# Performance work log

Measured on AMD Instinct MI355X. Metric: run time of the kernel, lower is better.

## Reference

```python
import jax, jax.numpy as jnp
import numpy as np

N_NODES = 10000
N_EDGES = 640000
IN_FEATS = 128
H_FEATS1 = 128
NUM_OUTPUTS = 64


def setup_inputs() -> dict:
    key = jax.random.key(0)
    k0, k1, k2, k3, k4 = jax.random.split(key, 5)
    in_feat = jax.random.normal(k0, (N_NODES, IN_FEATS), dtype=jnp.float32)
    src = jax.random.randint(k1, (N_EDGES,), 0, N_NODES, dtype=jnp.int64)
    dst = jax.random.randint(k2, (N_EDGES,), 0, N_NODES, dtype=jnp.int64)
    W1 = jax.random.normal(k3, (IN_FEATS, H_FEATS1), dtype=jnp.float32) * 0.05
    b1 = jnp.zeros((H_FEATS1,), dtype=jnp.float32)
    W2 = jax.random.normal(k4, (H_FEATS1, NUM_OUTPUTS), dtype=jnp.float32) * 0.05
    b2 = jnp.zeros((NUM_OUTPUTS,), dtype=jnp.float32)
    return {"in_feat": in_feat, "src": src, "dst": dst,
            "W1": W1, "b1": b1, "W2": W2, "b2": b2}


def _graph_conv(src, dst, x, W, b):
    # DGL GraphConv with norm='both': out = D_out^{-1/2} A^T-agg D_in^{-1/2} x W + b
    n = x.shape[0]
    ones = jnp.ones((src.shape[0],), dtype=x.dtype)
    deg_out = jnp.clip(jax.ops.segment_sum(ones, src, num_segments=n), 1.0)
    deg_in = jnp.clip(jax.ops.segment_sum(ones, dst, num_segments=n), 1.0)
    h = x * jax.lax.rsqrt(deg_out)[:, None]            # src-side normalization
    agg = jax.ops.segment_sum(h[src], dst, num_segments=n)  # SpMM: sum over in-edges
    agg = agg * jax.lax.rsqrt(deg_in)[:, None]         # dst-side normalization
    return agg @ W + b


def reference(in_feat, src, dst, W1, b1, W2, b2):
    h = _graph_conv(src, dst, in_feat, W1, b1)
    h = jax.nn.relu(h)  # dropout=0 -> identity
    return _graph_conv(src, dst, h, W2, b2)
```

## Files before the change

kernel.cpp:

```cpp
#include <hip/hip_runtime.h>
#include <hip/hip_fp16.h>

#define NFEAT 128
#define NOUT  64
#define PCAP  128
#define HB    256
#define NPB   16

__global__ void hist_kernel(const int* __restrict__ src, const int* __restrict__ dst,
                            unsigned char* __restrict__ hist_src,
                            unsigned char* __restrict__ hist_dst,
                            int nN, int nE) {
    extern __shared__ int bins[];
    int b = blockIdx.x;
    int per = (nE + HB - 1) / HB;
    int lo = b * per, hi = min(lo + per, nE);
    for (int i = threadIdx.x; i < nN; i += blockDim.x) bins[i] = 0;
    __syncthreads();
    for (int e = lo + threadIdx.x; e < hi; e += blockDim.x) {
        int s = src[e], d = dst[e];
        atomicAdd(&bins[d], 1);
        atomicAdd(&bins[s], 0x10000);
    }
    __syncthreads();
    for (int i = threadIdx.x; i < nN; i += blockDim.x) {
        int v = bins[i];
        hist_dst[(size_t)b * nN + i] = (unsigned char)min(v & 0xFFFF, 255);
        hist_src[(size_t)b * nN + i] = (unsigned char)min(v >> 16, 255);
    }
}

__global__ void offsets_kernel(const unsigned char* __restrict__ hist_src,
                               const unsigned char* __restrict__ hist_dst,
                               unsigned char* __restrict__ base_rel,
                               unsigned short* __restrict__ deg_in,
                               float* __restrict__ rs_in, float* __restrict__ rs_out, int nN) {
    int tid = blockIdx.x * blockDim.x + threadIdx.x;
    int wid = tid >> 6;
    int lane = tid & 63;
    int i0 = wid * 4;
    if (i0 >= nN) return;
    int c0 = lane * 4;
    unsigned int d[4], s4[4];
#pragma unroll
    for (int u = 0; u < 4; u++) {
        d[u]  = *(const unsigned int*)&hist_dst[(size_t)(c0 + u) * nN + i0];
        s4[u] = *(const unsigned int*)&hist_src[(size_t)(c0 + u) * nN + i0];
    }
    unsigned int run = 0, pre[4];
#pragma unroll
    for (int u = 0; u < 4; u++) { pre[u] = run; run += d[u]; }
    unsigned int ssum = s4[0] + s4[1] + s4[2] + s4[3];
    unsigned int inc = run;
#pragma unroll
    for (int off = 1; off < 64; off <<= 1) {
        unsigned int t = (unsigned int)__shfl_up((int)inc, off);
        if (lane >= off) inc += t;
    }
    unsigned int excl = inc - run;
#pragma unroll
    for (int u = 0; u < 4; u++)
        *(unsigned int*)&base_rel[(size_t)(c0 + u) * nN + i0] = excl + pre[u];
    unsigned int dtot = (unsigned int)__shfl((int)inc, 63);
#pragma unroll
    for (int off = 1; off < 64; off <<= 1)
        ssum += (unsigned int)__shfl_xor((int)ssum, off);
    if (lane < 4) {
        int i = i0 + lane;
        int dg = (dtot >> (8 * lane)) & 0xFF;
        int sg = (ssum >> (8 * lane)) & 0xFF;
        deg_in[i] = (unsigned short)min(dg, PCAP);
        rs_in[i]  = rsqrtf(fmaxf((float)dg, 1.0f));
        rs_out[i] = rsqrtf(fmaxf((float)sg, 1.0f));
    }
}

__global__ void scatter_kernel(const int* __restrict__ src, const int* __restrict__ dst,
                               const unsigned char* __restrict__ base_rel,
                               const float* __restrict__ x, const float* __restrict__ rs_out,
                               unsigned short* __restrict__ csr, uint4* __restrict__ xh,
                               int nN, int nE) {
    extern __shared__ int cur[];
    int b = blockIdx.x;
    int per = (nE + HB - 1) / HB;
    int lo = b * per, hi = min(lo + per, nE);
    for (int i = threadIdx.x; i < nN; i += blockDim.x)
        cur[i] = base_rel[(size_t)b * nN + i];
    __syncthreads();
    for (int e = lo + threadIdx.x; e < hi; e += blockDim.x) {
        int s = src[e], d = dst[e];
        int pos = atomicAdd(&cur[d], 1);
        if (pos < PCAP)
            csr[(size_t)d * PCAP + pos] = (unsigned short)s;
    }
    const float4* xf = (const float4*)x;
    int nchunk = nN * NFEAT / 8;
    for (int c = blockIdx.x * blockDim.x + threadIdx.x; c < nchunk; c += gridDim.x * blockDim.x) {
        int row = c >> 4;
        float rs = rs_out[row];
        float4 a = xf[2 * c], bb = xf[2 * c + 1];
        __half2 h[4] = {__floats2half2_rn(a.x * rs, a.y * rs),
                        __floats2half2_rn(a.z * rs, a.w * rs),
                        __floats2half2_rn(bb.x * rs, bb.y * rs),
                        __floats2half2_rn(bb.z * rs, bb.w * rs)};
        xh[c] = *(uint4*)h;
    }
}

__device__ __forceinline__ void add8(float* acc, uint4 v) {
    const __half2* h = (const __half2*)&v;
    float2 p0 = __half22float2(h[0]), p1 = __half22float2(h[1]);
    float2 p2 = __half22float2(h[2]), p3 = __half22float2(h[3]);
    acc[0] += p0.x; acc[1] += p0.y; acc[2] += p1.x; acc[3] += p1.y;
    acc[4] += p2.x; acc[5] += p2.y; acc[6] += p3.x; acc[7] += p3.y;
}

__global__ void gather_mlp_kernel(const unsigned short* __restrict__ deg_in,
                                  const unsigned short* __restrict__ csr,
                                  const uint4* __restrict__ xh,
                                  const float* __restrict__ rs_out,
                                  const float* __restrict__ rs_in,
                                  const float* __restrict__ W1, const float* __restrict__ b1,
                                  const float* __restrict__ W2, __half* __restrict__ zh,
                                  int nN) {
    __shared__ float ts[NPB][NFEAT];
    __shared__ float h1[NPB][NFEAT];
    __shared__ unsigned short eids[4][PCAP];
    int tid = threadIdx.x;
    int w = tid >> 6, lane = tid & 63;
    int i0 = blockIdx.x * NPB;
    int quad = lane >> 4;
    int g = lane & 15;

    for (int r = 0; r < 4; r++) {
        int node = w * 4 + r;
        int i = i0 + node;
        int n = deg_in[i];
        ((unsigned int*)eids[w])[lane] =
            ((const unsigned int*)(csr + (size_t)i * PCAP))[lane];
        __syncthreads();
        float s_in = rs_in[i];
        float acc[8] = {0.f, 0.f, 0.f, 0.f, 0.f, 0.f, 0.f, 0.f};
        int e = quad;
        for (; e + 28 < n; e += 32) {
            uint4 vv[8];
#pragma unroll
            for (int u = 0; u < 8; u++) {
                int s = eids[w][e + 4 * u];
                vv[u] = xh[(size_t)s * 16 + g];
            }
#pragma unroll
            for (int u = 0; u < 8; u++) add8(acc, vv[u]);
        }
        for (; e + 12 < n; e += 16) {
            uint4 vv[4];
#pragma unroll
            for (int u = 0; u < 4; u++) {
                int s = eids[w][e + 4 * u];
                vv[u] = xh[(size_t)s * 16 + g];
            }
#pragma unroll
            for (int u = 0; u < 4; u++) add8(acc, vv[u]);
        }
        for (; e < n; e += 4)
            add8(acc, xh[(size_t)eids[w][e] * 16 + g]);
#pragma unroll
        for (int d = 16; d <= 32; d <<= 1)
#pragma unroll
            for (int k = 0; k < 8; k++) acc[k] += __shfl_xor(acc[k], d);
        if (lane < 16) {
            float4 o0 = {acc[0] * s_in, acc[1] * s_in, acc[2] * s_in, acc[3] * s_in};
            float4 o1 = {acc[4] * s_in, acc[5] * s_in, acc[6] * s_in, acc[7] * s_in};
            float4* tp = (float4*)(&ts[node][g * 8]);
            tp[0] = o0; tp[1] = o1;
        }
        __syncthreads();
    }
    {
        int j = tid & 127;
        int gq = (tid >> 7) * 8;
        float a[8];
        float bb = b1[j];
#pragma unroll
        for (int u = 0; u < 8; u++) a[u] = bb;
#pragma unroll 8
        for (int k = 0; k < NFEAT; k++) {
            float wv = W1[k * NFEAT + j];
#pragma unroll
            for (int u = 0; u < 8; u++) a[u] += ts[gq + u][k] * wv;
        }
#pragma unroll
        for (int u = 0; u < 8; u++) h1[gq + u][j] = fmaxf(a[u], 0.0f);
    }
    __syncthreads();
    {
        int j2 = tid & 63;
        int g2 = (tid >> 6) * 4;
        float c[4] = {0.f, 0.f, 0.f, 0.f};
#pragma unroll 8
        for (int k = 0; k < NFEAT; k++) {
            float wv = W2[k * NOUT + j2];
#pragma unroll
            for (int u = 0; u < 4; u++) c[u] += h1[g2 + u][k] * wv;
        }
#pragma unroll
        for (int u = 0; u < 4; u++)
            zh[(size_t)(i0 + g2 + u) * NOUT + j2] =
                __float2half_rn(c[u] * rs_out[i0 + g2 + u]);
    }
}

__global__ void gather2_kernel(const unsigned short* __restrict__ deg_in,
                               const unsigned short* __restrict__ csr,
                               const uint4* __restrict__ zh, const float* __restrict__ rs_in,
                               const float* __restrict__ b2, float* __restrict__ out, int nN) {
    __shared__ unsigned short eids[4][PCAP];
    int tid = threadIdx.x;
    int w = tid >> 6, lane = tid & 63;
    int i = blockIdx.x * 4 + w;
    int n = deg_in[i];
    ((unsigned int*)eids[w])[lane] = ((const unsigned int*)(csr + (size_t)i * PCAP))[lane];

    int oct = lane >> 3;
    int g = lane & 7;
    float acc[8] = {0.f, 0.f, 0.f, 0.f, 0.f, 0.f, 0.f, 0.f};
    int e = oct;
    for (; e + 56 < n; e += 64) {
        uint4 vv[8];
#pragma unroll
        for (int u = 0; u < 8; u++) vv[u] = zh[(size_t)eids[w][e + 8 * u] * 8 + g];
#pragma unroll
        for (int u = 0; u < 8; u++) add8(acc, vv[u]);
    }
    for (; e + 24 < n; e += 32) {
        uint4 vv[4];
#pragma unroll
        for (int u = 0; u < 4; u++) vv[u] = zh[(size_t)eids[w][e + 8 * u] * 8 + g];
#pragma unroll
        for (int u = 0; u < 4; u++) add8(acc, vv[u]);
    }
    for (; e < n; e += 8)
        add8(acc, zh[(size_t)eids[w][e] * 8 + g]);
#pragma unroll
    for (int d = 8; d <= 32; d <<= 1)
#pragma unroll
        for (int k = 0; k < 8; k++) acc[k] += __shfl_xor(acc[k], d);
    if (lane < 8) {
        float s = rs_in[i];
        float4 bb0 = ((const float4*)b2)[2 * g], bb1 = ((const float4*)b2)[2 * g + 1];
        float4 o0 = {acc[0] * s + bb0.x, acc[1] * s + bb0.y, acc[2] * s + bb0.z, acc[3] * s + bb0.w};
        float4 o1 = {acc[4] * s + bb1.x, acc[5] * s + bb1.y, acc[6] * s + bb1.z, acc[7] * s + bb1.w};
        float4* op = (float4*)(out + (size_t)i * NOUT + g * 8);
        op[0] = o0; op[1] = o1;
    }
}

extern "C" void kernel_launch(void* const* d_in, const int* in_sizes, int n_in,
                              void* d_out, int out_size, void* d_ws, size_t ws_size,
                              hipStream_t stream) {
    const float* x  = (const float*)d_in[0];
    const int* src  = (const int*)d_in[1];
    const int* dst  = (const int*)d_in[2];
    const float* W1 = (const float*)d_in[3];
    const float* b1 = (const float*)d_in[4];
    const float* W2 = (const float*)d_in[5];
    const float* b2 = (const float*)d_in[6];
    float* out = (float*)d_out;

    const int nN = in_sizes[0] / NFEAT;
    const int nE = in_sizes[1];

    char* p = (char*)d_ws;
    uint4* xh = (uint4*)p;                        p += (size_t)nN * NFEAT * 2;
    unsigned char* hist_src = (unsigned char*)p;  p += (size_t)HB * nN;
    unsigned char* hist_dst = (unsigned char*)p;  p += (size_t)HB * nN;
    unsigned char* base_rel = (unsigned char*)p;  p += (size_t)HB * nN;
    unsigned short* csr     = (unsigned short*)p; p += (size_t)nN * PCAP * 2;
    unsigned short* deg_in  = (unsigned short*)p; p += (size_t)nN * 2;
    float* rs_in  = (float*)p; p += (size_t)nN * sizeof(float);
    float* rs_out = (float*)p; p += (size_t)nN * sizeof(float);
    __half* zh = (__half*)p;   p += (size_t)nN * NOUT * 2;

    hist_kernel<<<HB, 1024, (size_t)nN * sizeof(int), stream>>>(
        src, dst, hist_src, hist_dst, nN, nE);
    {
        int waves = nN / 4;
        int blocks = (waves * 64 + 255) / 256;
        offsets_kernel<<<blocks, 256, 0, stream>>>(
            hist_src, hist_dst, base_rel, deg_in, rs_in, rs_out, nN);
    }
    scatter_kernel<<<HB, 1024, (size_t)nN * sizeof(int), stream>>>(
        src, dst, base_rel, x, rs_out, csr, xh, nN, nE);
    gather_mlp_kernel<<<nN / NPB, 256, 0, stream>>>(
        deg_in, csr, xh, rs_out, rs_in, W1, b1, W2, zh, nN);
    gather2_kernel<<<nN / 4, 256, 0, stream>>>(
        deg_in, csr, (const uint4*)zh, rs_in, b2, out, nN);
}
```

Before: 136.2 us.

## Use one wave per node in gather_mlp with 1024-thread blocks

The gather+MLP kernel now launches 1024 threads per block, so each of the 16 waves handles one destination node at once. This replaces the loop over 4 nodes per wave, which had two block-wide barriers per iteration. The dense W1 and W2 stages now compute 2 nodes and 1 node per thread instead of 8 and 4. That gives more parallelism but less register reuse of each weight load and more weight loads per block. Larger blocks may also limit occupancy because of register and LDS use.

```diff
diff --git a/kernel.cpp b/kernel.cpp
--- a/kernel.cpp
+++ b/kernel.cpp
@@ -125,20 +125,18 @@
                                   int nN) {
     __shared__ float ts[NPB][NFEAT];
     __shared__ float h1[NPB][NFEAT];
-    __shared__ unsigned short eids[4][PCAP];
+    __shared__ unsigned short eids[NPB][PCAP];
     int tid = threadIdx.x;
     int w = tid >> 6, lane = tid & 63;
     int i0 = blockIdx.x * NPB;
+    int i = i0 + w;
     int quad = lane >> 4;
     int g = lane & 15;
 
-    for (int r = 0; r < 4; r++) {
-        int node = w * 4 + r;
-        int i = i0 + node;
+    {
         int n = deg_in[i];
         ((unsigned int*)eids[w])[lane] =
             ((const unsigned int*)(csr + (size_t)i * PCAP))[lane];
-        __syncthreads();
         float s_in = rs_in[i];
         float acc[8] = {0.f, 0.f, 0.f, 0.f, 0.f, 0.f, 0.f, 0.f};
         int e = quad;
@@ -171,42 +169,33 @@
         if (lane < 16) {
             float4 o0 = {acc[0] * s_in, acc[1] * s_in, acc[2] * s_in, acc[3] * s_in};
             float4 o1 = {acc[4] * s_in, acc[5] * s_in, acc[6] * s_in, acc[7] * s_in};
-            float4* tp = (float4*)(&ts[node][g * 8]);
+            float4* tp = (float4*)(&ts[w][g * 8]);
             tp[0] = o0; tp[1] = o1;
         }
-        __syncthreads();
-    }
+    }
+    __syncthreads();
     {
         int j = tid & 127;
-        int gq = (tid >> 7) * 8;
-        float a[8];
-        float bb = b1[j];
-#pragma unroll
-        for (int u = 0; u < 8; u++) a[u] = bb;
+        int gq = (tid >> 7) * 2;
+        float a0 = b1[j], a1 = a0;
 #pragma unroll 8
         for (int k = 0; k < NFEAT; k++) {
             float wv = W1[k * NFEAT + j];
-#pragma unroll
-            for (int u = 0; u < 8; u++) a[u] += ts[gq + u][k] * wv;
-        }
-#pragma unroll
-        for (int u = 0; u < 8; u++) h1[gq + u][j] = fmaxf(a[u], 0.0f);
+            a0 += ts[gq][k] * wv;
+            a1 += ts[gq + 1][k] * wv;
+        }
+        h1[gq][j] = fmaxf(a0, 0.0f);
+        h1[gq + 1][j] = fmaxf(a1, 0.0f);
     }
     __syncthreads();
     {
         int j2 = tid & 63;
-        int g2 = (tid >> 6) * 4;
-        float c[4] = {0.f, 0.f, 0.f, 0.f};
+        int n2 = tid >> 6;
+        float c = 0.f;
 #pragma unroll 8
-        for (int k = 0; k < NFEAT; k++) {
-            float wv = W2[k * NOUT + j2];
-#pragma unroll
-            for (int u = 0; u < 4; u++) c[u] += h1[g2 + u][k] * wv;
-        }
-#pragma unroll
-        for (int u = 0; u < 4; u++)
-            zh[(size_t)(i0 + g2 + u) * NOUT + j2] =
-                __float2half_rn(c[u] * rs_out[i0 + g2 + u]);
+        for (int k = 0; k < NFEAT; k++)
+            c += h1[n2][k] * W2[k * NOUT + j2];
+        zh[(size_t)(i0 + n2) * NOUT + j2] = __float2half_rn(c * rs_out[i0 + n2]);
     }
 }
 
@@ -291,7 +280,7 @@
     }
     scatter_kernel<<<HB, 1024, (size_t)nN * sizeof(int), stream>>>(
         src, dst, base_rel, x, rs_out, csr, xh, nN, nE);
-    gather_mlp_kernel<<<nN / NPB, 256, 0, stream>>>(
+    gather_mlp_kernel<<<nN / NPB, 1024, 0, stream>>>(
         deg_in, csr, xh, rs_out, rs_in, W1, b1, W2, zh, nN);
     gather2_kernel<<<nN / 4, 256, 0, stream>>>(
         deg_in, csr, (const uint4*)zh, rs_in, b2, out, nN);
```

Result: slower. 147.2 us (+8.1%).
